# Performance work log

Measured on AMD Instinct MI355X. Metric: run time of the kernel, lower is better.

The kernel has to match this reference:

```python
import jax, jax.numpy as jnp
import numpy as np

# Hard-coded 36-node detector graph from the source (1-indexed), 220 directed edges.
E_SRC = [1,2,3,4,5,6,7,8,9,10,11,12,13,14,15,16,17,18,19,20,21,22,23,24,25,26,27,28,29,30,31,32,33,34,35,36,4,3,8,7,19,20,15,16,35,36,31,32,11,12,11,11,11,12,12,12,6,5,25,26,28,25,9,9,9,10,10,10,1,2,3,4,5,6,7,8,9,10,11,12,13,14,15,16,17,18,17,18,19,20,16,15,31,32,36,35,3,4,7,8,6,5,25,28,14,9,12,11,1,4,2,3,4,1,6,7,8,5,10,11,12,9,14,15,16,13,18,19,20,17,22,23,24,21,26,27,28,25,30,31,32,29,34,35,36,33,33,34,1,2,14,13,30,29,23,22,21,24,22,21,36,33,4,31,30,15,27,28,18,17,10,9,14,19,18,5,8,1,19,20,21,22,23,24,25,26,27,28,29,30,31,32,33,34,35,36,25,26,13,14,30,29,24,21,23,22,33,34,1,2,28,27,10,9,12,15,22,21,11,10]
E_DST = [2,3,4,1,6,7,8,5,10,11,12,9,14,15,16,13,18,19,20,17,22,23,24,21,26,27,28,25,30,31,32,29,34,35,36,33,33,34,1,2,14,13,30,29,23,22,21,24,22,21,36,33,4,31,30,15,27,28,18,17,10,9,14,19,18,5,8,1,19,20,21,22,23,24,25,26,27,28,29,30,31,32,33,34,35,36,25,26,13,14,30,29,24,21,23,22,33,34,1,2,28,27,10,9,12,15,22,21,11,10,1,2,3,4,5,6,7,8,9,10,11,12,13,14,15,16,17,18,19,20,21,22,23,24,25,26,27,28,29,30,31,32,33,34,35,36,4,3,8,7,19,20,15,16,35,36,31,32,11,12,11,11,11,12,12,12,6,5,25,26,28,25,9,9,9,10,10,10,1,2,3,4,5,6,7,8,9,10,11,12,13,14,15,16,17,18,17,18,19,20,16,15,31,32,36,35,3,4,7,8,6,5,25,28,14,9,12,11,1,4]

B = 20000   # graphs per batch
P = 36      # nodes per graph
N = B * P


def setup_inputs() -> dict:
    key = jax.random.key(0)
    ks = jax.random.split(key, 12)
    src = np.asarray(E_SRC, np.int32) - 1
    dst = np.asarray(E_DST, np.int32) - 1
    offs = (np.arange(B, dtype=np.int32) * P)[:, None]
    edge_index = jnp.asarray(np.stack([(src[None, :] + offs).reshape(-1),
                                       (dst[None, :] + offs).reshape(-1)]))  # [2, B*220]
    batch_index = jnp.asarray(np.repeat(np.arange(B, dtype=np.int32), P))  # [N]
    x = jax.random.normal(ks[0], (N, 2), jnp.float32)
    pos = jax.random.normal(ks[1], (N, 3), jnp.float32)  # unused by forward (faithful to source)

    def lin_w(k, fi, fo):
        s = 1.0 / np.sqrt(fi)
        return jax.random.uniform(k, (fi, fo), jnp.float32, -s, s)

    def lin_b(k, fo):
        return jax.random.uniform(k, (fo,), jnp.float32, -0.05, 0.05)

    return {
        "x": x, "edge_index": edge_index, "pos": pos, "batch_index": batch_index,
        "W0": lin_w(ks[2], 2, 4),   "b0": lin_b(ks[3], 4),
        "W1": lin_w(ks[4], 4, 12),  "b1": lin_b(ks[5], 12),
        "W2": lin_w(ks[6], 12, 16), "b2": lin_b(ks[7], 16),
        "W3": lin_w(ks[8], 16, 32), "b3": lin_b(ks[9], 32),
        "Wfc": lin_w(ks[10], 64, 7), "bfc": lin_b(ks[11], 7),
    }


def reference(x, edge_index, pos, batch_index, W0, b0, W1, b1, W2, b2, W3, b3, Wfc, bfc):
    del pos  # present in the torch signature but unused
    src, dst = edge_index[0], edge_index[1]
    n = x.shape[0]
    # GCN symmetric normalization with self-loops: deg = 1 + in-degree
    deg = jax.ops.segment_sum(jnp.ones(src.shape, x.dtype), dst, num_segments=n) + 1.0
    inv = deg ** -0.5
    enorm = inv[src] * inv[dst]   # edge norm
    snorm = inv * inv             # self-loop norm (deg^-1)

    def gcn_conv(h, W, b):
        h = h @ W  # [n, fo]
        agg = jax.ops.segment_sum(h[src] * enorm[:, None], dst, num_segments=n)
        return agg + h * snorm[:, None] + b

    h = jax.nn.relu(gcn_conv(x, W0, b0))
    h = jax.nn.relu(gcn_conv(h, W1, b1))
    # dropout(0.2) is identity in eval mode
    h = jax.nn.relu(gcn_conv(h, W2, b2))
    h = jax.nn.relu(gcn_conv(h, W3, b3))

    gmp = jax.ops.segment_max(h, batch_index, num_segments=B)
    counts = jax.ops.segment_sum(jnp.ones((n,), h.dtype), batch_index, num_segments=B)
    gap = jax.ops.segment_sum(h, batch_index, num_segments=B) / counts[:, None]
    hidden = jnp.concatenate([gmp, gap], axis=1)  # [B, 64]
    out = jax.nn.relu(hidden @ Wfc + bfc)         # [B, 7]
    return (out, hidden)
```

## Files before the change

### kernel.cpp

```cpp
#include <hip/hip_runtime.h>

typedef __attribute__((ext_vector_type(2))) float f32x2;
typedef __attribute__((ext_vector_type(4))) float f32x4;

#define NGRAPH 20000
#define GPB 6
#define STRIDE 36
#define SB (STRIDE * 4)
#define BOFF 64

static __constant__ int c_indeg[36] = {
    7,5,5,7,6,5,5,6,9,9,9,9,5,7,7,5,5,6,6,5,7,7,5,5,7,5,5,7,5,6,6,5,6,5,5,6
};
static __constant__ signed char c_adj[36][9] = {
    {3,7,9,6,1,18,10,0,0},      {0,6,7,2,19,0,0,0,0},
    {1,3,33,32,20,0,0,0,0},     {2,10,0,32,21,33,9,0,0},
    {7,9,5,27,22,26,0,0,0},     {4,6,26,23,27,0,0,0,0},
    {5,7,1,24,0,0,0,0,0},       {6,9,4,0,25,1,0,0,0},
    {11,24,27,9,13,18,17,26,14},{8,27,24,3,10,4,7,0,27},
    {9,0,11,21,35,32,3,28,20},  {10,13,8,20,30,29,14,29,21},
    {15,19,18,13,30,0,0,0,0},   {12,18,8,19,14,31,11,0,0},
    {13,11,8,15,29,32,28,0,0},  {14,12,28,33,29,0,0,0,0},
    {19,25,17,34,24,0,0,0,0},   {16,24,8,18,35,25,0,0,0},
    {17,8,0,19,13,12,0,0,0},    {18,1,16,12,13,0,0,0,0},
    {23,30,11,2,31,10,21,0,0},  {20,35,10,3,34,11,22,0,0},
    {21,34,4,35,23,0,0,0,0},    {22,31,5,30,20,0,0,0,0},
    {27,6,16,25,17,8,9,0,0},    {24,7,17,26,16,0,0,0,0},
    {25,5,8,27,4,0,0,0,0},      {26,4,9,5,24,9,8,0,0},
    {31,15,10,14,29,0,0,0,0},   {28,14,11,11,15,30,0,0,0},
    {29,11,12,31,20,23,0,0,0},  {30,13,28,23,20,0,0,0,0},
    {35,3,10,14,2,33,0,0,0},    {32,2,15,3,34,0,0,0,0},
    {33,16,35,22,21,0,0,0,0},   {34,10,17,32,21,22,0,0,0},
};
static __constant__ float c_inv[36] = {
    0.35355339f,0.40824829f,0.40824829f,0.35355339f,0.37796447f,0.40824829f,
    0.40824829f,0.37796447f,0.31622777f,0.31622777f,0.31622777f,0.31622777f,
    0.40824829f,0.35355339f,0.35355339f,0.40824829f,0.40824829f,0.37796447f,
    0.37796447f,0.40824829f,0.35355339f,0.35355339f,0.40824829f,0.40824829f,
    0.35355339f,0.40824829f,0.40824829f,0.35355339f,0.40824829f,0.37796447f,
    0.37796447f,0.40824829f,0.37796447f,0.40824829f,0.40824829f,0.37796447f,
};

static __device__ __forceinline__ f32x2 relu2(f32x2 v) {
    return __builtin_elementwise_max(v, (f32x2){0.f, 0.f});
}

extern "C" __global__ __launch_bounds__(256, 5)
void gcn_fused(const float* __restrict__ x,
               const float* __restrict__ W0, const float* __restrict__ b0,
               const float* __restrict__ W1, const float* __restrict__ b1,
               const float* __restrict__ W2, const float* __restrict__ b2,
               const float* __restrict__ W3, const float* __restrict__ b3,
               const float* __restrict__ Wfc, const float* __restrict__ bfc,
               float* __restrict__ out)
{
    __shared__ float L[GPB * 36 * STRIDE];

    const int t = threadIdx.x;
    const int g = t / 36;
    const int v = t - g * 36;
    const bool act = (g < GPB);
    const int gq = act ? g : GPB - 1;
    const int vc = act ? v : 0;
    const int G  = blockIdx.x * GPB + g;
    const int Gc = (act && G < NGRAPH) ? G : 0;

    const int nd = c_indeg[vc];
    const float inv_v = c_inv[vc];
    int aoff[9];
#pragma unroll
    for (int k = 0; k < 9; ++k)
        aoff[k] = (gq * 36 + (int)c_adj[vc][k]) * SB;
    float* srow = &L[(gq * 36 + vc) * STRIDE];
    const char* Lb = (const char*)L;

    f32x2 h0a, h0b;
    {
        const float2 xv = ((const float2*)x)[(size_t)Gc * 36 + vc];
        const float s0 = xv.x * inv_v, s1 = xv.y * inv_v;
        if (act) { srow[0] = s0; srow[1] = s1; }
        __syncthreads();
        f32x2 c = {s0, s1};
#pragma unroll
        for (int k = 0; k < 5; ++k) c += *(const f32x2*)(Lb + aoff[k]);
        if (nd > 5) c += *(const f32x2*)(Lb + aoff[5]);
        if (nd > 6) c += *(const f32x2*)(Lb + aoff[6]);
        if (nd > 7) { c += *(const f32x2*)(Lb + aoff[7]);
                      c += *(const f32x2*)(Lb + aoff[8]); }
        const float a0 = c.x * inv_v, a1 = c.y * inv_v;
        const f32x2 a0v = {a0, a0}, a1v = {a1, a1};
        const f32x2* W0v = (const f32x2*)W0;
        const f32x2* b0v = (const f32x2*)b0;
        h0a = relu2(__builtin_elementwise_fma(a0v, W0v[0],
                    __builtin_elementwise_fma(a1v, W0v[2], b0v[0])));
        h0b = relu2(__builtin_elementwise_fma(a0v, W0v[1],
                    __builtin_elementwise_fma(a1v, W0v[3], b0v[1])));
    }

    f32x2 h1[6];
    {
        const f32x2 iv = {inv_v, inv_v};
        const f32x2 s0 = h0a * iv, s1 = h0b * iv;
        if (act) *(f32x4*)&srow[16] = (f32x4){s0.x, s0.y, s1.x, s1.y};
        __syncthreads();
        f32x4 c = {s0.x, s0.y, s1.x, s1.y};
#pragma unroll
        for (int k = 0; k < 5; ++k) c += *(const f32x4*)(Lb + aoff[k] + BOFF);
        if (nd > 5) c += *(const f32x4*)(Lb + aoff[5] + BOFF);
        if (nd > 6) c += *(const f32x4*)(Lb + aoff[6] + BOFF);
        if (nd > 7) { c += *(const f32x4*)(Lb + aoff[7] + BOFF);
                      c += *(const f32x4*)(Lb + aoff[8] + BOFF); }
        float a[4];
#pragma unroll
        for (int i = 0; i < 4; ++i) a[i] = c[i] * inv_v;
        f32x2 z[6];
        const f32x2* b1v = (const f32x2*)b1;
#pragma unroll
        for (int j = 0; j < 6; ++j) z[j] = b1v[j];
        const f32x2* W1v = (const f32x2*)W1;
#pragma unroll
        for (int i = 0; i < 4; ++i) {
            const f32x2 av = {a[i], a[i]};
#pragma unroll
            for (int j = 0; j < 6; ++j)
                z[j] = __builtin_elementwise_fma(av, W1v[i * 6 + j], z[j]);
        }
#pragma unroll
        for (int j = 0; j < 6; ++j) h1[j] = relu2(z[j]);
    }

    f32x2 h2[8];
    {
        const f32x2 iv = {inv_v, inv_v};
        f32x2 s[6];
#pragma unroll
        for (int j = 0; j < 6; ++j) s[j] = h1[j] * iv;
        if (act) {
            *(f32x4*)&srow[0] = (f32x4){s[0].x, s[0].y, s[1].x, s[1].y};
            *(f32x4*)&srow[4] = (f32x4){s[2].x, s[2].y, s[3].x, s[3].y};
            *(f32x4*)&srow[8] = (f32x4){s[4].x, s[4].y, s[5].x, s[5].y};
        }
        __syncthreads();
        f32x4 c0 = {s[0].x, s[0].y, s[1].x, s[1].y};
        f32x4 c1 = {s[2].x, s[2].y, s[3].x, s[3].y};
        f32x4 c2 = {s[4].x, s[4].y, s[5].x, s[5].y};
#pragma unroll
        for (int k = 0; k < 5; ++k) {
            const char* base = Lb + aoff[k];
            c0 += *(const f32x4*)(base);
            c1 += *(const f32x4*)(base + 16);
            c2 += *(const f32x4*)(base + 32);
        }
        if (nd > 5) { const char* base = Lb + aoff[5];
            c0 += *(const f32x4*)(base); c1 += *(const f32x4*)(base + 16);
            c2 += *(const f32x4*)(base + 32); }
        if (nd > 6) { const char* base = Lb + aoff[6];
            c0 += *(const f32x4*)(base); c1 += *(const f32x4*)(base + 16);
            c2 += *(const f32x4*)(base + 32); }
        if (nd > 7) {
            const char* ba = Lb + aoff[7];
            c0 += *(const f32x4*)(ba); c1 += *(const f32x4*)(ba + 16);
            c2 += *(const f32x4*)(ba + 32);
            const char* bb = Lb + aoff[8];
            c0 += *(const f32x4*)(bb); c1 += *(const f32x4*)(bb + 16);
            c2 += *(const f32x4*)(bb + 32);
        }
        float a[12];
#pragma unroll
        for (int i = 0; i < 4; ++i) {
            a[i] = c0[i] * inv_v; a[4 + i] = c1[i] * inv_v; a[8 + i] = c2[i] * inv_v;
        }
        f32x2 z[8];
        const f32x2* b2v = (const f32x2*)b2;
#pragma unroll
        for (int j = 0; j < 8; ++j) z[j] = b2v[j];
        const f32x2* W2v = (const f32x2*)W2;
#pragma unroll
        for (int i = 0; i < 12; ++i) {
            const f32x2 av = {a[i], a[i]};
#pragma unroll
            for (int j = 0; j < 8; ++j)
                z[j] = __builtin_elementwise_fma(av, W2v[i * 8 + j], z[j]);
        }
#pragma unroll
        for (int j = 0; j < 8; ++j) h2[j] = relu2(z[j]);
    }

    f32x2 h3[16];
    {
        const f32x2 iv = {inv_v, inv_v};
        f32x2 s[8];
#pragma unroll
        for (int j = 0; j < 8; ++j) s[j] = h2[j] * iv;
        if (act) {
#pragma unroll
            for (int q = 0; q < 4; ++q)
                *(f32x4*)&srow[16 + q * 4] =
                    (f32x4){s[2*q].x, s[2*q].y, s[2*q+1].x, s[2*q+1].y};
        }
        __syncthreads();
        f32x4 c0 = {s[0].x, s[0].y, s[1].x, s[1].y};
        f32x4 c1 = {s[2].x, s[2].y, s[3].x, s[3].y};
        f32x4 c2 = {s[4].x, s[4].y, s[5].x, s[5].y};
        f32x4 c3 = {s[6].x, s[6].y, s[7].x, s[7].y};
#pragma unroll
        for (int k = 0; k < 5; ++k) {
            const char* base = Lb + aoff[k] + BOFF;
            c0 += *(const f32x4*)(base);      c1 += *(const f32x4*)(base + 16);
            c2 += *(const f32x4*)(base + 32); c3 += *(const f32x4*)(base + 48);
        }
        if (nd > 5) { const char* base = Lb + aoff[5] + BOFF;
            c0 += *(const f32x4*)(base);      c1 += *(const f32x4*)(base + 16);
            c2 += *(const f32x4*)(base + 32); c3 += *(const f32x4*)(base + 48); }
        if (nd > 6) { const char* base = Lb + aoff[6] + BOFF;
            c0 += *(const f32x4*)(base);      c1 += *(const f32x4*)(base + 16);
            c2 += *(const f32x4*)(base + 32); c3 += *(const f32x4*)(base + 48); }
        if (nd > 7) {
            const char* ba = Lb + aoff[7] + BOFF;
            c0 += *(const f32x4*)(ba);      c1 += *(const f32x4*)(ba + 16);
            c2 += *(const f32x4*)(ba + 32); c3 += *(const f32x4*)(ba + 48);
            const char* bb = Lb + aoff[8] + BOFF;
            c0 += *(const f32x4*)(bb);      c1 += *(const f32x4*)(bb + 16);
            c2 += *(const f32x4*)(bb + 32); c3 += *(const f32x4*)(bb + 48);
        }
        float a[16];
#pragma unroll
        for (int i = 0; i < 4; ++i) {
            a[i] = c0[i] * inv_v;      a[4 + i] = c1[i] * inv_v;
            a[8 + i] = c2[i] * inv_v;  a[12 + i] = c3[i] * inv_v;
        }
        f32x2 z[16];
        const f32x2* b3v = (const f32x2*)b3;
#pragma unroll
        for (int j = 0; j < 16; ++j) z[j] = b3v[j];
        const f32x2* W3v = (const f32x2*)W3;
#pragma unroll
        for (int i = 0; i < 16; ++i) {
            const f32x2 av = {a[i], a[i]};
#pragma unroll
            for (int j = 0; j < 16; ++j)
                z[j] = __builtin_elementwise_fma(av, W3v[i * 16 + j], z[j]);
        }
#pragma unroll
        for (int j = 0; j < 16; ++j) h3[j] = relu2(z[j]);
    }

    if (act) {
#pragma unroll
        for (int q = 0; q < 4; ++q)
            *(f32x4*)&srow[q * 4] =
                (f32x4){h3[2*q].x, h3[2*q].y, h3[2*q+1].x, h3[2*q+1].y};
    }
    __syncthreads();
    if (act) {
#pragma unroll
        for (int q = 0; q < 4; ++q)
            *(f32x4*)&srow[16 + q * 4] =
                (f32x4){h3[8+2*q].x, h3[8+2*q].y, h3[9+2*q].x, h3[9+2*q].y};
    }
    __syncthreads();

    if (t < GPB * 32) {
        const int pg = t >> 5, pf = t & 31;
        const int PG = blockIdx.x * GPB + pg;
        const float* col = &L[(pg * 36) * STRIDE + pf];
        float mx = -1e30f, sm = 0.f;
#pragma unroll
        for (int u = 0; u < 36; ++u) {
            const float val = col[u * STRIDE];
            mx = fmaxf(mx, val); sm += val;
        }
        const float gap = sm * (1.0f / 36.0f);
        if (PG < NGRAPH) {
            float* ho = out + (size_t)NGRAPH * 7 + (size_t)PG * 64;
            ho[pf] = mx; ho[32 + pf] = gap;
        }
        float p[7];
        const float* wr0 = Wfc + pf * 7;
        const float* wr1 = Wfc + (32 + pf) * 7;
#pragma unroll
        for (int o = 0; o < 7; ++o)
            p[o] = fmaf(mx, wr0[o], gap * wr1[o]);
#pragma unroll
        for (int m = 16; m >= 1; m >>= 1) {
#pragma unroll
            for (int o = 0; o < 7; ++o)
                p[o] += __shfl_xor(p[o], m, 32);
        }
        if (pf < 7 && PG < NGRAPH) {
            float w = p[0];
            w = (pf == 1) ? p[1] : w;
            w = (pf == 2) ? p[2] : w;
            w = (pf == 3) ? p[3] : w;
            w = (pf == 4) ? p[4] : w;
            w = (pf == 5) ? p[5] : w;
            w = (pf == 6) ? p[6] : w;
            out[(size_t)PG * 7 + pf] = fmaxf(w + bfc[pf], 0.f);
        }
    }
}

extern "C" void kernel_launch(void* const* d_in, const int* in_sizes, int n_in,
                              void* d_out, int out_size, void* d_ws, size_t ws_size,
                              hipStream_t stream) {
    (void)in_sizes; (void)n_in; (void)d_ws; (void)ws_size; (void)out_size;
    const float* x   = (const float*)d_in[0];
    const float* W0  = (const float*)d_in[4];
    const float* b0  = (const float*)d_in[5];
    const float* W1  = (const float*)d_in[6];
    const float* b1  = (const float*)d_in[7];
    const float* W2  = (const float*)d_in[8];
    const float* b2  = (const float*)d_in[9];
    const float* W3  = (const float*)d_in[10];
    const float* b3  = (const float*)d_in[11];
    const float* Wfc = (const float*)d_in[12];
    const float* bfc = (const float*)d_in[13];
    float* out = (float*)d_out;

    const int nblocks = (NGRAPH + GPB - 1) / GPB;
    hipLaunchKernelGGL(gcn_fused, dim3(nblocks), dim3(256), 0, stream,
                       x, W0, b0, W1, b1, W2, b2, W3, b3, Wfc, bfc, out);
}
```

Before: 35.77 us.

## Pack seven graphs per block and aggregate layer 0 from global memory

Each block now handles seven graphs (252 of 256 threads) instead of six, and the launch-bounds occupancy hint drops from 5 to 4. The first layer's neighbour aggregation now reads the neighbours' x values straight from global memory with a per-edge precomputed normalisation table. This removes one LDS write and one barrier. The shared-memory column offsets are reshuffled to match, the adjacency row is loaded as packed words, and the pooling loop is unrolled by two. In exchange the kernel does more scattered global loads, and the lower occupancy hint may limit latency hiding.

```diff
diff --git a/kernel.cpp b/kernel.cpp
--- a/kernel.cpp
+++ b/kernel.cpp
@@ -4,10 +4,9 @@
 typedef __attribute__((ext_vector_type(4))) float f32x4;
 
 #define NGRAPH 20000
-#define GPB 6
+#define GPB 7
 #define STRIDE 36
 #define SB (STRIDE * 4)
-#define BOFF 64
 
 static __constant__ int c_indeg[36] = {
     7,5,5,7,6,5,5,6,9,9,9,9,5,7,7,5,5,6,6,5,7,7,5,5,7,5,5,7,5,6,6,5,6,5,5,6
@@ -40,12 +39,36 @@
     0.35355339f,0.40824829f,0.40824829f,0.35355339f,0.40824829f,0.37796447f,
     0.37796447f,0.40824829f,0.37796447f,0.40824829f,0.40824829f,0.37796447f,
 };
+#define A_ 0.35355339f
+#define B_ 0.40824829f
+#define C_ 0.37796447f
+#define D_ 0.31622777f
+static __constant__ float c_ninv[36][9] = {
+    {A_,C_,D_,B_,B_,C_,D_,0,0}, {A_,B_,C_,B_,B_,0,0,0,0},
+    {B_,A_,B_,C_,A_,0,0,0,0},   {B_,D_,A_,C_,A_,B_,D_,0,0},
+    {C_,D_,B_,A_,B_,B_,0,0,0},  {C_,B_,B_,B_,A_,0,0,0,0},
+    {B_,C_,B_,A_,A_,0,0,0,0},   {B_,D_,C_,A_,B_,B_,0,0,0},
+    {D_,A_,A_,D_,A_,C_,C_,B_,A_},{D_,A_,A_,A_,D_,C_,C_,A_,A_},
+    {D_,A_,D_,A_,C_,C_,A_,B_,A_},{D_,A_,D_,A_,C_,C_,A_,C_,A_},
+    {B_,B_,C_,A_,C_,0,0,0,0},   {B_,C_,D_,B_,A_,B_,D_,0,0},
+    {A_,D_,D_,B_,C_,C_,B_,0,0}, {A_,B_,B_,B_,C_,0,0,0,0},
+    {B_,B_,C_,B_,A_,0,0,0,0},   {B_,A_,D_,C_,C_,B_,0,0,0},
+    {C_,D_,A_,B_,A_,B_,0,0,0},  {C_,B_,B_,B_,A_,0,0,0,0},
+    {B_,C_,D_,B_,B_,D_,A_,0,0}, {A_,C_,D_,A_,B_,D_,B_,0,0},
+    {A_,B_,C_,C_,B_,0,0,0,0},   {B_,B_,B_,C_,A_,0,0,0,0},
+    {A_,B_,B_,B_,C_,D_,D_,0,0}, {A_,C_,C_,B_,B_,0,0,0,0},
+    {B_,B_,D_,A_,C_,0,0,0,0},   {B_,C_,D_,B_,A_,D_,D_,0,0},
+    {B_,B_,D_,A_,C_,0,0,0,0},   {B_,A_,D_,D_,B_,C_,0,0,0},
+    {C_,D_,B_,B_,A_,B_,0,0,0},  {C_,A_,B_,B_,A_,0,0,0,0},
+    {C_,A_,D_,A_,B_,B_,0,0,0},  {C_,B_,B_,A_,B_,0,0,0,0},
+    {B_,B_,C_,B_,A_,0,0,0,0},   {B_,D_,C_,C_,A_,B_,0,0,0},
+};
 
 static __device__ __forceinline__ f32x2 relu2(f32x2 v) {
     return __builtin_elementwise_max(v, (f32x2){0.f, 0.f});
 }
 
-extern "C" __global__ __launch_bounds__(256, 5)
+extern "C" __global__ __launch_bounds__(256, 4)
 void gcn_fused(const float* __restrict__ x,
                const float* __restrict__ W0, const float* __restrict__ b0,
                const float* __restrict__ W1, const float* __restrict__ b1,
@@ -67,27 +90,47 @@
 
     const int nd = c_indeg[vc];
     const float inv_v = c_inv[vc];
-    int aoff[9];
-#pragma unroll
-    for (int k = 0; k < 9; ++k)
-        aoff[k] = (gq * 36 + (int)c_adj[vc][k]) * SB;
+    int nb[9], aoff[9];
+    {
+        const unsigned char* ar = (const unsigned char*)&c_adj[vc][0];
+        const unsigned int w0 = *(const unsigned int*)(ar);
+        const unsigned int w1 = *(const unsigned int*)(ar + 4);
+        const unsigned int w2 = *(const unsigned int*)(ar + 8);
+#pragma unroll
+        for (int k = 0; k < 4; ++k) nb[k] = (int)((w0 >> (8 * k)) & 0xff);
+#pragma unroll
+        for (int k = 0; k < 4; ++k) nb[4 + k] = (int)((w1 >> (8 * k)) & 0xff);
+        nb[8] = (int)(w2 & 0xff);
+#pragma unroll
+        for (int k = 0; k < 9; ++k) aoff[k] = (gq * 36 + nb[k]) * SB;
+    }
     float* srow = &L[(gq * 36 + vc) * STRIDE];
     const char* Lb = (const char*)L;
 
     f32x2 h0a, h0b;
     {
-        const float2 xv = ((const float2*)x)[(size_t)Gc * 36 + vc];
-        const float s0 = xv.x * inv_v, s1 = xv.y * inv_v;
-        if (act) { srow[0] = s0; srow[1] = s1; }
-        __syncthreads();
-        f32x2 c = {s0, s1};
-#pragma unroll
-        for (int k = 0; k < 5; ++k) c += *(const f32x2*)(Lb + aoff[k]);
-        if (nd > 5) c += *(const f32x2*)(Lb + aoff[5]);
-        if (nd > 6) c += *(const f32x2*)(Lb + aoff[6]);
-        if (nd > 7) { c += *(const f32x2*)(Lb + aoff[7]);
-                      c += *(const f32x2*)(Lb + aoff[8]); }
-        const float a0 = c.x * inv_v, a1 = c.y * inv_v;
+        const float2* x2 = (const float2*)x;
+        const int xb = Gc * 36;
+        const float2 xs = x2[xb + vc];
+        f32x2 acc = {xs.x * inv_v, xs.y * inv_v};
+        const float* nr = &c_ninv[vc][0];
+#pragma unroll
+        for (int k = 0; k < 5; ++k) {
+            const float2 xu = x2[xb + nb[k]];
+            const float w = nr[k];
+            acc.x = fmaf(w, xu.x, acc.x); acc.y = fmaf(w, xu.y, acc.y);
+        }
+        if (nd > 5) { const float2 xu = x2[xb + nb[5]]; const float w = nr[5];
+            acc.x = fmaf(w, xu.x, acc.x); acc.y = fmaf(w, xu.y, acc.y); }
+        if (nd > 6) { const float2 xu = x2[xb + nb[6]]; const float w = nr[6];
+            acc.x = fmaf(w, xu.x, acc.x); acc.y = fmaf(w, xu.y, acc.y); }
+        if (nd > 7) {
+            const float2 xu7 = x2[xb + nb[7]]; const float w7 = nr[7];
+            acc.x = fmaf(w7, xu7.x, acc.x); acc.y = fmaf(w7, xu7.y, acc.y);
+            const float2 xu8 = x2[xb + nb[8]]; const float w8 = nr[8];
+            acc.x = fmaf(w8, xu8.x, acc.x); acc.y = fmaf(w8, xu8.y, acc.y);
+        }
+        const float a0 = acc.x * inv_v, a1 = acc.y * inv_v;
         const f32x2 a0v = {a0, a0}, a1v = {a1, a1};
         const f32x2* W0v = (const f32x2*)W0;
         const f32x2* b0v = (const f32x2*)b0;
@@ -101,15 +144,15 @@
     {
         const f32x2 iv = {inv_v, inv_v};
         const f32x2 s0 = h0a * iv, s1 = h0b * iv;
-        if (act) *(f32x4*)&srow[16] = (f32x4){s0.x, s0.y, s1.x, s1.y};
+        if (act) *(f32x4*)&srow[0] = (f32x4){s0.x, s0.y, s1.x, s1.y};
         __syncthreads();
         f32x4 c = {s0.x, s0.y, s1.x, s1.y};
 #pragma unroll
-        for (int k = 0; k < 5; ++k) c += *(const f32x4*)(Lb + aoff[k] + BOFF);
-        if (nd > 5) c += *(const f32x4*)(Lb + aoff[5] + BOFF);
-        if (nd > 6) c += *(const f32x4*)(Lb + aoff[6] + BOFF);
-        if (nd > 7) { c += *(const f32x4*)(Lb + aoff[7] + BOFF);
-                      c += *(const f32x4*)(Lb + aoff[8] + BOFF); }
+        for (int k = 0; k < 5; ++k) c += *(const f32x4*)(Lb + aoff[k]);
+        if (nd > 5) c += *(const f32x4*)(Lb + aoff[5]);
+        if (nd > 6) c += *(const f32x4*)(Lb + aoff[6]);
+        if (nd > 7) { c += *(const f32x4*)(Lb + aoff[7]);
+                      c += *(const f32x4*)(Lb + aoff[8]); }
         float a[4];
 #pragma unroll
         for (int i = 0; i < 4; ++i) a[i] = c[i] * inv_v;
@@ -136,9 +179,9 @@
 #pragma unroll
         for (int j = 0; j < 6; ++j) s[j] = h1[j] * iv;
         if (act) {
-            *(f32x4*)&srow[0] = (f32x4){s[0].x, s[0].y, s[1].x, s[1].y};
-            *(f32x4*)&srow[4] = (f32x4){s[2].x, s[2].y, s[3].x, s[3].y};
-            *(f32x4*)&srow[8] = (f32x4){s[4].x, s[4].y, s[5].x, s[5].y};
+            *(f32x4*)&srow[4]  = (f32x4){s[0].x, s[0].y, s[1].x, s[1].y};
+            *(f32x4*)&srow[8]  = (f32x4){s[2].x, s[2].y, s[3].x, s[3].y};
+            *(f32x4*)&srow[12] = (f32x4){s[4].x, s[4].y, s[5].x, s[5].y};
         }
         __syncthreads();
         f32x4 c0 = {s[0].x, s[0].y, s[1].x, s[1].y};
@@ -146,22 +189,22 @@
         f32x4 c2 = {s[4].x, s[4].y, s[5].x, s[5].y};
 #pragma unroll
         for (int k = 0; k < 5; ++k) {
-            const char* base = Lb + aoff[k];
+            const char* base = Lb + aoff[k] + 16;
             c0 += *(const f32x4*)(base);
             c1 += *(const f32x4*)(base + 16);
             c2 += *(const f32x4*)(base + 32);
         }
-        if (nd > 5) { const char* base = Lb + aoff[5];
+        if (nd > 5) { const char* base = Lb + aoff[5] + 16;
             c0 += *(const f32x4*)(base); c1 += *(const f32x4*)(base + 16);
             c2 += *(const f32x4*)(base + 32); }
-        if (nd > 6) { const char* base = Lb + aoff[6];
+        if (nd > 6) { const char* base = Lb + aoff[6] + 16;
             c0 += *(const f32x4*)(base); c1 += *(const f32x4*)(base + 16);
             c2 += *(const f32x4*)(base + 32); }
         if (nd > 7) {
-            const char* ba = Lb + aoff[7];
+            const char* ba = Lb + aoff[7] + 16;
             c0 += *(const f32x4*)(ba); c1 += *(const f32x4*)(ba + 16);
             c2 += *(const f32x4*)(ba + 32);
-            const char* bb = Lb + aoff[8];
+            const char* bb = Lb + aoff[8] + 16;
             c0 += *(const f32x4*)(bb); c1 += *(const f32x4*)(bb + 16);
             c2 += *(const f32x4*)(bb + 32);
         }
@@ -205,21 +248,21 @@
         f32x4 c3 = {s[6].x, s[6].y, s[7].x, s[7].y};
 #pragma unroll
         for (int k = 0; k < 5; ++k) {
-            const char* base = Lb + aoff[k] + BOFF;
+            const char* base = Lb + aoff[k] + 64;
             c0 += *(const f32x4*)(base);      c1 += *(const f32x4*)(base + 16);
             c2 += *(const f32x4*)(base + 32); c3 += *(const f32x4*)(base + 48);
         }
-        if (nd > 5) { const char* base = Lb + aoff[5] + BOFF;
+        if (nd > 5) { const char* base = Lb + aoff[5] + 64;
             c0 += *(const f32x4*)(base);      c1 += *(const f32x4*)(base + 16);
             c2 += *(const f32x4*)(base + 32); c3 += *(const f32x4*)(base + 48); }
-        if (nd > 6) { const char* base = Lb + aoff[6] + BOFF;
+        if (nd > 6) { const char* base = Lb + aoff[6] + 64;
             c0 += *(const f32x4*)(base);      c1 += *(const f32x4*)(base + 16);
             c2 += *(const f32x4*)(base + 32); c3 += *(const f32x4*)(base + 48); }
         if (nd > 7) {
-            const char* ba = Lb + aoff[7] + BOFF;
+            const char* ba = Lb + aoff[7] + 64;
             c0 += *(const f32x4*)(ba);      c1 += *(const f32x4*)(ba + 16);
             c2 += *(const f32x4*)(ba + 32); c3 += *(const f32x4*)(ba + 48);
-            const char* bb = Lb + aoff[8] + BOFF;
+            const char* bb = Lb + aoff[8] + 64;
             c0 += *(const f32x4*)(bb);      c1 += *(const f32x4*)(bb + 16);
             c2 += *(const f32x4*)(bb + 32); c3 += *(const f32x4*)(bb + 48);
         }
@@ -266,9 +309,10 @@
         const float* col = &L[(pg * 36) * STRIDE + pf];
         float mx = -1e30f, sm = 0.f;
 #pragma unroll
-        for (int u = 0; u < 36; ++u) {
-            const float val = col[u * STRIDE];
-            mx = fmaxf(mx, val); sm += val;
+        for (int u = 0; u < 18; ++u) {
+            const float v0 = col[0], v1 = col[STRIDE];
+            mx = fmaxf(mx, fmaxf(v0, v1)); sm += v0 + v1;
+            col += 2 * STRIDE;
         }
         const float gap = sm * (1.0f / 36.0f);
         if (PG < NGRAPH) {
```

New measurement: 36.40 us. No clear change (+1.7%).

## Process two interleaved graph streams per thread with seven graphs per stream

Applied to the files above, without the earlier changes.

Each thread now handles one node in two separate graphs (stream A and stream B), and each block packs 7 graphs per stream instead of 6, so every block covers 14 graphs. This raises thread utilization (252 of 256 threads active) and gives each thread independent instruction streams to hide LDS and FMA latency. Weight loads are now shared across the two graphs. The cost is doubled register and LDS use per block, with launch bounds lowered to 2 blocks per CU, so occupancy drops. The LDS row layout is also reshuffled to fit the larger feature slices.

```diff
diff --git a/kernel.cpp b/kernel.cpp
--- a/kernel.cpp
+++ b/kernel.cpp
@@ -4,10 +4,11 @@
 typedef __attribute__((ext_vector_type(4))) float f32x4;
 
 #define NGRAPH 20000
-#define GPB 6
+#define GPT 7
 #define STRIDE 36
 #define SB (STRIDE * 4)
-#define BOFF 64
+#define BSTREAM (GPT * 36 * STRIDE)
+#define BSTREAMB (BSTREAM * 4)
 
 static __constant__ int c_indeg[36] = {
     7,5,5,7,6,5,5,6,9,9,9,9,5,7,7,5,5,6,6,5,7,7,5,5,7,5,5,7,5,6,6,5,6,5,5,6
@@ -45,7 +46,59 @@
     return __builtin_elementwise_max(v, (f32x2){0.f, 0.f});
 }
 
-extern "C" __global__ __launch_bounds__(256, 5)
+static __device__ __forceinline__ void xf1(const float* a, const float* W1,
+                                           const float* b1, f32x2* h) {
+    f32x2 z[6];
+    const f32x2* bv = (const f32x2*)b1;
+#pragma unroll
+    for (int j = 0; j < 6; ++j) z[j] = bv[j];
+    const f32x2* Wv = (const f32x2*)W1;
+#pragma unroll
+    for (int i = 0; i < 4; ++i) {
+        const f32x2 av = {a[i], a[i]};
+#pragma unroll
+        for (int j = 0; j < 6; ++j)
+            z[j] = __builtin_elementwise_fma(av, Wv[i * 6 + j], z[j]);
+    }
+#pragma unroll
+    for (int j = 0; j < 6; ++j) h[j] = relu2(z[j]);
+}
+static __device__ __forceinline__ void xf2(const float* a, const float* W2,
+                                           const float* b2, f32x2* h) {
+    f32x2 z[8];
+    const f32x2* bv = (const f32x2*)b2;
+#pragma unroll
+    for (int j = 0; j < 8; ++j) z[j] = bv[j];
+    const f32x2* Wv = (const f32x2*)W2;
+#pragma unroll
+    for (int i = 0; i < 12; ++i) {
+        const f32x2 av = {a[i], a[i]};
+#pragma unroll
+        for (int j = 0; j < 8; ++j)
+            z[j] = __builtin_elementwise_fma(av, Wv[i * 8 + j], z[j]);
+    }
+#pragma unroll
+    for (int j = 0; j < 8; ++j) h[j] = relu2(z[j]);
+}
+static __device__ __forceinline__ void xf3(const float* a, const float* W3,
+                                           const float* b3, f32x2* h) {
+    f32x2 z[16];
+    const f32x2* bv = (const f32x2*)b3;
+#pragma unroll
+    for (int j = 0; j < 16; ++j) z[j] = bv[j];
+    const f32x2* Wv = (const f32x2*)W3;
+#pragma unroll
+    for (int i = 0; i < 16; ++i) {
+        const f32x2 av = {a[i], a[i]};
+#pragma unroll
+        for (int j = 0; j < 16; ++j)
+            z[j] = __builtin_elementwise_fma(av, Wv[i * 16 + j], z[j]);
+    }
+#pragma unroll
+    for (int j = 0; j < 16; ++j) h[j] = relu2(z[j]);
+}
+
+extern "C" __global__ __launch_bounds__(256, 2)
 void gcn_fused(const float* __restrict__ x,
                const float* __restrict__ W0, const float* __restrict__ b0,
                const float* __restrict__ W1, const float* __restrict__ b1,
@@ -54,248 +107,302 @@
                const float* __restrict__ Wfc, const float* __restrict__ bfc,
                float* __restrict__ out)
 {
-    __shared__ float L[GPB * 36 * STRIDE];
+    __shared__ float L[2 * BSTREAM];
 
     const int t = threadIdx.x;
     const int g = t / 36;
     const int v = t - g * 36;
-    const bool act = (g < GPB);
-    const int gq = act ? g : GPB - 1;
+    const bool act = (g < GPT);
+    const int gq = act ? g : GPT - 1;
     const int vc = act ? v : 0;
-    const int G  = blockIdx.x * GPB + g;
-    const int Gc = (act && G < NGRAPH) ? G : 0;
+    const int GA = blockIdx.x * (2 * GPT) + g;
+    const int GB = GA + GPT;
+    const int GcA = (act && GA < NGRAPH) ? GA : 0;
+    const int GcB = (act && GB < NGRAPH) ? GB : 0;
+    const bool okB = (GB < NGRAPH);
 
     const int nd = c_indeg[vc];
     const float inv_v = c_inv[vc];
-    int aoff[9];
-#pragma unroll
-    for (int k = 0; k < 9; ++k)
+    int aoff[9], boff[9];
+#pragma unroll
+    for (int k = 0; k < 9; ++k) {
         aoff[k] = (gq * 36 + (int)c_adj[vc][k]) * SB;
-    float* srow = &L[(gq * 36 + vc) * STRIDE];
+        boff[k] = aoff[k] + BSTREAMB;
+    }
+    float* srowA = &L[(gq * 36 + vc) * STRIDE];
+    float* srowB = srowA + BSTREAM;
     const char* Lb = (const char*)L;
 
-    f32x2 h0a, h0b;
+    f32x2 h0A[2], h0B[2];
     {
-        const float2 xv = ((const float2*)x)[(size_t)Gc * 36 + vc];
-        const float s0 = xv.x * inv_v, s1 = xv.y * inv_v;
-        if (act) { srow[0] = s0; srow[1] = s1; }
+        const float2* x2 = (const float2*)x;
+        const float2 xA = x2[(size_t)GcA * 36 + vc];
+        const float2 xB = x2[(size_t)GcB * 36 + vc];
+        const f32x2 sA = {xA.x * inv_v, xA.y * inv_v};
+        const f32x2 sB = {xB.x * inv_v, xB.y * inv_v};
+        if (act) { *(f32x2*)&srowA[32] = sA; *(f32x2*)&srowB[32] = sB; }
         __syncthreads();
-        f32x2 c = {s0, s1};
-#pragma unroll
-        for (int k = 0; k < 5; ++k) c += *(const f32x2*)(Lb + aoff[k]);
-        if (nd > 5) c += *(const f32x2*)(Lb + aoff[5]);
-        if (nd > 6) c += *(const f32x2*)(Lb + aoff[6]);
-        if (nd > 7) { c += *(const f32x2*)(Lb + aoff[7]);
-                      c += *(const f32x2*)(Lb + aoff[8]); }
-        const float a0 = c.x * inv_v, a1 = c.y * inv_v;
-        const f32x2 a0v = {a0, a0}, a1v = {a1, a1};
+        f32x2 cA = sA, cB = sB;
+#pragma unroll
+        for (int k = 0; k < 5; ++k) {
+            cA += *(const f32x2*)(Lb + aoff[k] + 128);
+            cB += *(const f32x2*)(Lb + boff[k] + 128);
+        }
+        if (nd > 5) { cA += *(const f32x2*)(Lb + aoff[5] + 128);
+                      cB += *(const f32x2*)(Lb + boff[5] + 128); }
+        if (nd > 6) { cA += *(const f32x2*)(Lb + aoff[6] + 128);
+                      cB += *(const f32x2*)(Lb + boff[6] + 128); }
+        if (nd > 7) { cA += *(const f32x2*)(Lb + aoff[7] + 128);
+                      cB += *(const f32x2*)(Lb + boff[7] + 128);
+                      cA += *(const f32x2*)(Lb + aoff[8] + 128);
+                      cB += *(const f32x2*)(Lb + boff[8] + 128); }
         const f32x2* W0v = (const f32x2*)W0;
         const f32x2* b0v = (const f32x2*)b0;
-        h0a = relu2(__builtin_elementwise_fma(a0v, W0v[0],
-                    __builtin_elementwise_fma(a1v, W0v[2], b0v[0])));
-        h0b = relu2(__builtin_elementwise_fma(a0v, W0v[1],
-                    __builtin_elementwise_fma(a1v, W0v[3], b0v[1])));
-    }
-
-    f32x2 h1[6];
+        {
+            const float a0 = cA.x * inv_v, a1 = cA.y * inv_v;
+            const f32x2 a0v = {a0, a0}, a1v = {a1, a1};
+            h0A[0] = relu2(__builtin_elementwise_fma(a0v, W0v[0],
+                     __builtin_elementwise_fma(a1v, W0v[2], b0v[0])));
+            h0A[1] = relu2(__builtin_elementwise_fma(a0v, W0v[1],
+                     __builtin_elementwise_fma(a1v, W0v[3], b0v[1])));
+        }
+        {
+            const float a0 = cB.x * inv_v, a1 = cB.y * inv_v;
+            const f32x2 a0v = {a0, a0}, a1v = {a1, a1};
+            h0B[0] = relu2(__builtin_elementwise_fma(a0v, W0v[0],
+                     __builtin_elementwise_fma(a1v, W0v[2], b0v[0])));
+            h0B[1] = relu2(__builtin_elementwise_fma(a0v, W0v[1],
+                     __builtin_elementwise_fma(a1v, W0v[3], b0v[1])));
+        }
+    }
+
+    f32x2 h1A[6], h1B[6];
     {
         const f32x2 iv = {inv_v, inv_v};
-        const f32x2 s0 = h0a * iv, s1 = h0b * iv;
-        if (act) *(f32x4*)&srow[16] = (f32x4){s0.x, s0.y, s1.x, s1.y};
+        const f32x2 sA0 = h0A[0] * iv, sA1 = h0A[1] * iv;
+        const f32x2 sB0 = h0B[0] * iv, sB1 = h0B[1] * iv;
+        if (act) {
+            *(f32x4*)&srowA[0] = (f32x4){sA0.x, sA0.y, sA1.x, sA1.y};
+            *(f32x4*)&srowB[0] = (f32x4){sB0.x, sB0.y, sB1.x, sB1.y};
+        }
         __syncthreads();
-        f32x4 c = {s0.x, s0.y, s1.x, s1.y};
-#pragma unroll
-        for (int k = 0; k < 5; ++k) c += *(const f32x4*)(Lb + aoff[k] + BOFF);
-        if (nd > 5) c += *(const f32x4*)(Lb + aoff[5] + BOFF);
-        if (nd > 6) c += *(const f32x4*)(Lb + aoff[6] + BOFF);
-        if (nd > 7) { c += *(const f32x4*)(Lb + aoff[7] + BOFF);
-                      c += *(const f32x4*)(Lb + aoff[8] + BOFF); }
-        float a[4];
-#pragma unroll
-        for (int i = 0; i < 4; ++i) a[i] = c[i] * inv_v;
-        f32x2 z[6];
-        const f32x2* b1v = (const f32x2*)b1;
-#pragma unroll
-        for (int j = 0; j < 6; ++j) z[j] = b1v[j];
-        const f32x2* W1v = (const f32x2*)W1;
-#pragma unroll
-        for (int i = 0; i < 4; ++i) {
-            const f32x2 av = {a[i], a[i]};
-#pragma unroll
-            for (int j = 0; j < 6; ++j)
-                z[j] = __builtin_elementwise_fma(av, W1v[i * 6 + j], z[j]);
-        }
-#pragma unroll
-        for (int j = 0; j < 6; ++j) h1[j] = relu2(z[j]);
-    }
-
-    f32x2 h2[8];
+        f32x4 cA = {sA0.x, sA0.y, sA1.x, sA1.y};
+        f32x4 cB = {sB0.x, sB0.y, sB1.x, sB1.y};
+#pragma unroll
+        for (int k = 0; k < 5; ++k) {
+            cA += *(const f32x4*)(Lb + aoff[k]);
+            cB += *(const f32x4*)(Lb + boff[k]);
+        }
+        if (nd > 5) { cA += *(const f32x4*)(Lb + aoff[5]);
+                      cB += *(const f32x4*)(Lb + boff[5]); }
+        if (nd > 6) { cA += *(const f32x4*)(Lb + aoff[6]);
+                      cB += *(const f32x4*)(Lb + boff[6]); }
+        if (nd > 7) { cA += *(const f32x4*)(Lb + aoff[7]);
+                      cB += *(const f32x4*)(Lb + boff[7]);
+                      cA += *(const f32x4*)(Lb + aoff[8]);
+                      cB += *(const f32x4*)(Lb + boff[8]); }
+        float aA[4], aB[4];
+#pragma unroll
+        for (int i = 0; i < 4; ++i) { aA[i] = cA[i] * inv_v; aB[i] = cB[i] * inv_v; }
+        xf1(aA, W1, b1, h1A);
+        xf1(aB, W1, b1, h1B);
+    }
+
+    f32x2 h2A[8], h2B[8];
     {
         const f32x2 iv = {inv_v, inv_v};
-        f32x2 s[6];
-#pragma unroll
-        for (int j = 0; j < 6; ++j) s[j] = h1[j] * iv;
+        f32x2 sA[6], sB[6];
+#pragma unroll
+        for (int j = 0; j < 6; ++j) { sA[j] = h1A[j] * iv; sB[j] = h1B[j] * iv; }
         if (act) {
-            *(f32x4*)&srow[0] = (f32x4){s[0].x, s[0].y, s[1].x, s[1].y};
-            *(f32x4*)&srow[4] = (f32x4){s[2].x, s[2].y, s[3].x, s[3].y};
-            *(f32x4*)&srow[8] = (f32x4){s[4].x, s[4].y, s[5].x, s[5].y};
+            *(f32x4*)&srowA[4]  = (f32x4){sA[0].x, sA[0].y, sA[1].x, sA[1].y};
+            *(f32x4*)&srowA[8]  = (f32x4){sA[2].x, sA[2].y, sA[3].x, sA[3].y};
+            *(f32x4*)&srowA[12] = (f32x4){sA[4].x, sA[4].y, sA[5].x, sA[5].y};
+            *(f32x4*)&srowB[4]  = (f32x4){sB[0].x, sB[0].y, sB[1].x, sB[1].y};
+            *(f32x4*)&srowB[8]  = (f32x4){sB[2].x, sB[2].y, sB[3].x, sB[3].y};
+            *(f32x4*)&srowB[12] = (f32x4){sB[4].x, sB[4].y, sB[5].x, sB[5].y};
         }
         __syncthreads();
-        f32x4 c0 = {s[0].x, s[0].y, s[1].x, s[1].y};
-        f32x4 c1 = {s[2].x, s[2].y, s[3].x, s[3].y};
-        f32x4 c2 = {s[4].x, s[4].y, s[5].x, s[5].y};
+        f32x4 cA0 = {sA[0].x, sA[0].y, sA[1].x, sA[1].y};
+        f32x4 cA1 = {sA[2].x, sA[2].y, sA[3].x, sA[3].y};
+        f32x4 cA2 = {sA[4].x, sA[4].y, sA[5].x, sA[5].y};
+        f32x4 cB0 = {sB[0].x, sB[0].y, sB[1].x, sB[1].y};
+        f32x4 cB1 = {sB[2].x, sB[2].y, sB[3].x, sB[3].y};
+        f32x4 cB2 = {sB[4].x, sB[4].y, sB[5].x, sB[5].y};
 #pragma unroll
         for (int k = 0; k < 5; ++k) {
-            const char* base = Lb + aoff[k];
-            c0 += *(const f32x4*)(base);
-            c1 += *(const f32x4*)(base + 16);
-            c2 += *(const f32x4*)(base + 32);
-        }
-        if (nd > 5) { const char* base = Lb + aoff[5];
-            c0 += *(const f32x4*)(base); c1 += *(const f32x4*)(base + 16);
-            c2 += *(const f32x4*)(base + 32); }
-        if (nd > 6) { const char* base = Lb + aoff[6];
-            c0 += *(const f32x4*)(base); c1 += *(const f32x4*)(base + 16);
-            c2 += *(const f32x4*)(base + 32); }
+            const char* pa = Lb + aoff[k] + 16;
+            const char* pb = Lb + boff[k] + 16;
+            cA0 += *(const f32x4*)(pa);      cB0 += *(const f32x4*)(pb);
+            cA1 += *(const f32x4*)(pa + 16); cB1 += *(const f32x4*)(pb + 16);
+            cA2 += *(const f32x4*)(pa + 32); cB2 += *(const f32x4*)(pb + 32);
+        }
+        if (nd > 5) { const char* pa = Lb + aoff[5] + 16; const char* pb = Lb + boff[5] + 16;
+            cA0 += *(const f32x4*)(pa);      cB0 += *(const f32x4*)(pb);
+            cA1 += *(const f32x4*)(pa + 16); cB1 += *(const f32x4*)(pb + 16);
+            cA2 += *(const f32x4*)(pa + 32); cB2 += *(const f32x4*)(pb + 32); }
+        if (nd > 6) { const char* pa = Lb + aoff[6] + 16; const char* pb = Lb + boff[6] + 16;
+            cA0 += *(const f32x4*)(pa);      cB0 += *(const f32x4*)(pb);
+            cA1 += *(const f32x4*)(pa + 16); cB1 += *(const f32x4*)(pb + 16);
+            cA2 += *(const f32x4*)(pa + 32); cB2 += *(const f32x4*)(pb + 32); }
         if (nd > 7) {
-            const char* ba = Lb + aoff[7];
-            c0 += *(const f32x4*)(ba); c1 += *(const f32x4*)(ba + 16);
-            c2 += *(const f32x4*)(ba + 32);
-            const char* bb = Lb + aoff[8];
-            c0 += *(const f32x4*)(bb); c1 += *(const f32x4*)(bb + 16);
-            c2 += *(const f32x4*)(bb + 32);
-        }
-        float a[12];
+            const char* pa = Lb + aoff[7] + 16; const char* pb = Lb + boff[7] + 16;
+            cA0 += *(const f32x4*)(pa);      cB0 += *(const f32x4*)(pb);
+            cA1 += *(const f32x4*)(pa + 16); cB1 += *(const f32x4*)(pb + 16);
+            cA2 += *(const f32x4*)(pa + 32); cB2 += *(const f32x4*)(pb + 32);
+            const char* qa = Lb + aoff[8] + 16; const char* qb = Lb + boff[8] + 16;
+            cA0 += *(const f32x4*)(qa);      cB0 += *(const f32x4*)(qb);
+            cA1 += *(const f32x4*)(qa + 16); cB1 += *(const f32x4*)(qb + 16);
+            cA2 += *(const f32x4*)(qa + 32); cB2 += *(const f32x4*)(qb + 32);
+        }
+        float aA[12], aB[12];
 #pragma unroll
         for (int i = 0; i < 4; ++i) {
-            a[i] = c0[i] * inv_v; a[4 + i] = c1[i] * inv_v; a[8 + i] = c2[i] * inv_v;
-        }
-        f32x2 z[8];
-        const f32x2* b2v = (const f32x2*)b2;
-#pragma unroll
-        for (int j = 0; j < 8; ++j) z[j] = b2v[j];
-        const f32x2* W2v = (const f32x2*)W2;
-#pragma unroll
-        for (int i = 0; i < 12; ++i) {
-            const f32x2 av = {a[i], a[i]};
-#pragma unroll
-            for (int j = 0; j < 8; ++j)
-                z[j] = __builtin_elementwise_fma(av, W2v[i * 8 + j], z[j]);
-        }
-#pragma unroll
-        for (int j = 0; j < 8; ++j) h2[j] = relu2(z[j]);
-    }
-
-    f32x2 h3[16];
+            aA[i] = cA0[i] * inv_v; aA[4+i] = cA1[i] * inv_v; aA[8+i] = cA2[i] * inv_v;
+            aB[i] = cB0[i] * inv_v; aB[4+i] = cB1[i] * inv_v; aB[8+i] = cB2[i] * inv_v;
+        }
+        xf2(aA, W2, b2, h2A);
+        xf2(aB, W2, b2, h2B);
+    }
+
+    f32x2 h3A[16], h3B[16];
     {
         const f32x2 iv = {inv_v, inv_v};
-        f32x2 s[8];
-#pragma unroll
-        for (int j = 0; j < 8; ++j) s[j] = h2[j] * iv;
+        f32x2 sA[8], sB[8];
+#pragma unroll
+        for (int j = 0; j < 8; ++j) { sA[j] = h2A[j] * iv; sB[j] = h2B[j] * iv; }
         if (act) {
 #pragma unroll
-            for (int q = 0; q < 4; ++q)
-                *(f32x4*)&srow[16 + q * 4] =
-                    (f32x4){s[2*q].x, s[2*q].y, s[2*q+1].x, s[2*q+1].y};
+            for (int q = 0; q < 4; ++q) {
+                *(f32x4*)&srowA[16 + q*4] =
+                    (f32x4){sA[2*q].x, sA[2*q].y, sA[2*q+1].x, sA[2*q+1].y};
+                *(f32x4*)&srowB[16 + q*4] =
+                    (f32x4){sB[2*q].x, sB[2*q].y, sB[2*q+1].x, sB[2*q+1].y};
+            }
         }
         __syncthreads();
-        f32x4 c0 = {s[0].x, s[0].y, s[1].x, s[1].y};
-        f32x4 c1 = {s[2].x, s[2].y, s[3].x, s[3].y};
-        f32x4 c2 = {s[4].x, s[4].y, s[5].x, s[5].y};
-        f32x4 c3 = {s[6].x, s[6].y, s[7].x, s[7].y};
+        f32x4 cA0 = {sA[0].x, sA[0].y, sA[1].x, sA[1].y};
+        f32x4 cA1 = {sA[2].x, sA[2].y, sA[3].x, sA[3].y};
+        f32x4 cA2 = {sA[4].x, sA[4].y, sA[5].x, sA[5].y};
+        f32x4 cA3 = {sA[6].x, sA[6].y, sA[7].x, sA[7].y};
+        f32x4 cB0 = {sB[0].x, sB[0].y, sB[1].x, sB[1].y};
+        f32x4 cB1 = {sB[2].x, sB[2].y, sB[3].x, sB[3].y};
+        f32x4 cB2 = {sB[4].x, sB[4].y, sB[5].x, sB[5].y};
+        f32x4 cB3 = {sB[6].x, sB[6].y, sB[7].x, sB[7].y};
 #pragma unroll
         for (int k = 0; k < 5; ++k) {
-            const char* base = Lb + aoff[k] + BOFF;
-            c0 += *(const f32x4*)(base);      c1 += *(const f32x4*)(base + 16);
-            c2 += *(const f32x4*)(base + 32); c3 += *(const f32x4*)(base + 48);
-        }
-        if (nd > 5) { const char* base = Lb + aoff[5] + BOFF;
-            c0 += *(const f32x4*)(base);      c1 += *(const f32x4*)(base + 16);
-            c2 += *(const f32x4*)(base + 32); c3 += *(const f32x4*)(base + 48); }
-        if (nd > 6) { const char* base = Lb + aoff[6] + BOFF;
-            c0 += *(const f32x4*)(base);      c1 += *(const f32x4*)(base + 16);
-            c2 += *(const f32x4*)(base + 32); c3 += *(const f32x4*)(base + 48); }
+            const char* pa = Lb + aoff[k] + 64;
+            const char* pb = Lb + boff[k] + 64;
+            cA0 += *(const f32x4*)(pa);      cB0 += *(const f32x4*)(pb);
+            cA1 += *(const f32x4*)(pa + 16); cB1 += *(const f32x4*)(pb + 16);
+            cA2 += *(const f32x4*)(pa + 32); cB2 += *(const f32x4*)(pb + 32);
+            cA3 += *(const f32x4*)(pa + 48); cB3 += *(const f32x4*)(pb + 48);
+        }
+        if (nd > 5) { const char* pa = Lb + aoff[5] + 64; const char* pb = Lb + boff[5] + 64;
+            cA0 += *(const f32x4*)(pa);      cB0 += *(const f32x4*)(pb);
+            cA1 += *(const f32x4*)(pa + 16); cB1 += *(const f32x4*)(pb + 16);
+            cA2 += *(const f32x4*)(pa + 32); cB2 += *(const f32x4*)(pb + 32);
+            cA3 += *(const f32x4*)(pa + 48); cB3 += *(const f32x4*)(pb + 48); }
+        if (nd > 6) { const char* pa = Lb + aoff[6] + 64; const char* pb = Lb + boff[6] + 64;
+            cA0 += *(const f32x4*)(pa);      cB0 += *(const f32x4*)(pb);
+            cA1 += *(const f32x4*)(pa + 16); cB1 += *(const f32x4*)(pb + 16);
+            cA2 += *(const f32x4*)(pa + 32); cB2 += *(const f32x4*)(pb + 32);
+            cA3 += *(const f32x4*)(pa + 48); cB3 += *(const f32x4*)(pb + 48); }
         if (nd > 7) {
-            const char* ba = Lb + aoff[7] + BOFF;
-            c0 += *(const f32x4*)(ba);      c1 += *(const f32x4*)(ba + 16);
-            c2 += *(const f32x4*)(ba + 32); c3 += *(const f32x4*)(ba + 48);
-            const char* bb = Lb + aoff[8] + BOFF;
-            c0 += *(const f32x4*)(bb);      c1 += *(const f32x4*)(bb + 16);
-            c2 += *(const f32x4*)(bb + 32); c3 += *(const f32x4*)(bb + 48);
-        }
-        float a[16];
+            const char* pa = Lb + aoff[7] + 64; const char* pb = Lb + boff[7] + 64;
+            cA0 += *(const f32x4*)(pa);      cB0 += *(const f32x4*)(pb);
+            cA1 += *(const f32x4*)(pa + 16); cB1 += *(const f32x4*)(pb + 16);
+            cA2 += *(const f32x4*)(pa + 32); cB2 += *(const f32x4*)(pb + 32);
+            cA3 += *(const f32x4*)(pa + 48); cB3 += *(const f32x4*)(pb + 48);
+            const char* qa = Lb + aoff[8] + 64; const char* qb = Lb + boff[8] + 64;
+            cA0 += *(const f32x4*)(qa);      cB0 += *(const f32x4*)(qb);
+            cA1 += *(const f32x4*)(qa + 16); cB1 += *(const f32x4*)(qb + 16);
+            cA2 += *(const f32x4*)(qa + 32); cB2 += *(const f32x4*)(qb + 32);
+            cA3 += *(const f32x4*)(qa + 48); cB3 += *(const f32x4*)(qb + 48);
+        }
+        float aA[16], aB[16];
 #pragma unroll
         for (int i = 0; i < 4; ++i) {
-            a[i] = c0[i] * inv_v;      a[4 + i] = c1[i] * inv_v;
-            a[8 + i] = c2[i] * inv_v;  a[12 + i] = c3[i] * inv_v;
-        }
-        f32x2 z[16];
-        const f32x2* b3v = (const f32x2*)b3;
-#pragma unroll
-        for (int j = 0; j < 16; ++j) z[j] = b3v[j];
-        const f32x2* W3v = (const f32x2*)W3;
-#pragma unroll
-        for (int i = 0; i < 16; ++i) {
-            const f32x2 av = {a[i], a[i]};
-#pragma unroll
-            for (int j = 0; j < 16; ++j)
-                z[j] = __builtin_elementwise_fma(av, W3v[i * 16 + j], z[j]);
-        }
-#pragma unroll
-        for (int j = 0; j < 16; ++j) h3[j] = relu2(z[j]);
+            aA[i] = cA0[i] * inv_v; aA[4+i]  = cA1[i] * inv_v;
+            aA[8+i] = cA2[i] * inv_v; aA[12+i] = cA3[i] * inv_v;
+            aB[i] = cB0[i] * inv_v; aB[4+i]  = cB1[i] * inv_v;
+            aB[8+i] = cB2[i] * inv_v; aB[12+i] = cB3[i] * inv_v;
+        }
+        xf3(aA, W3, b3, h3A);
+        xf3(aB, W3, b3, h3B);
     }
 
     if (act) {
-#pragma unroll
-        for (int q = 0; q < 4; ++q)
-            *(f32x4*)&srow[q * 4] =
-                (f32x4){h3[2*q].x, h3[2*q].y, h3[2*q+1].x, h3[2*q+1].y};
+        *(f32x4*)&srowA[0] = (f32x4){h3A[0].x, h3A[0].y, h3A[1].x, h3A[1].y};
+        *(f32x4*)&srowA[4] = (f32x4){h3A[2].x, h3A[2].y, h3A[3].x, h3A[3].y};
+        *(f32x4*)&srowA[8] = (f32x4){h3A[4].x, h3A[4].y, h3A[5].x, h3A[5].y};
+        *(f32x4*)&srowB[0] = (f32x4){h3B[0].x, h3B[0].y, h3B[1].x, h3B[1].y};
+        *(f32x4*)&srowB[4] = (f32x4){h3B[2].x, h3B[2].y, h3B[3].x, h3B[3].y};
+        *(f32x4*)&srowB[8] = (f32x4){h3B[4].x, h3B[4].y, h3B[5].x, h3B[5].y};
     }
     __syncthreads();
     if (act) {
 #pragma unroll
-        for (int q = 0; q < 4; ++q)
-            *(f32x4*)&srow[16 + q * 4] =
-                (f32x4){h3[8+2*q].x, h3[8+2*q].y, h3[9+2*q].x, h3[9+2*q].y};
+        for (int q = 0; q < 5; ++q) {
+            *(f32x4*)&srowA[12 + q*4] =
+                (f32x4){h3A[6+2*q].x, h3A[6+2*q].y, h3A[7+2*q].x, h3A[7+2*q].y};
+            *(f32x4*)&srowB[12 + q*4] =
+                (f32x4){h3B[6+2*q].x, h3B[6+2*q].y, h3B[7+2*q].x, h3B[7+2*q].y};
+        }
     }
     __syncthreads();
 
-    if (t < GPB * 32) {
+    if (t < GPT * 32) {
         const int pg = t >> 5, pf = t & 31;
-        const int PG = blockIdx.x * GPB + pg;
-        const float* col = &L[(pg * 36) * STRIDE + pf];
-        float mx = -1e30f, sm = 0.f;
+        const int PA = blockIdx.x * (2 * GPT) + pg;
+        const int PB = PA + GPT;
+        const float* colA = &L[(pg * 36) * STRIDE + pf];
+        const float* colB = colA + BSTREAM;
+        float mxA = -1e30f, smA = 0.f, mxB = -1e30f, smB = 0.f;
 #pragma unroll
         for (int u = 0; u < 36; ++u) {
-            const float val = col[u * STRIDE];
-            mx = fmaxf(mx, val); sm += val;
-        }
-        const float gap = sm * (1.0f / 36.0f);
-        if (PG < NGRAPH) {
-            float* ho = out + (size_t)NGRAPH * 7 + (size_t)PG * 64;
-            ho[pf] = mx; ho[32 + pf] = gap;
-        }
-        float p[7];
+            const float vA = colA[u * STRIDE];
+            const float vB = colB[u * STRIDE];
+            mxA = fmaxf(mxA, vA); smA += vA;
+            mxB = fmaxf(mxB, vB); smB += vB;
+        }
+        const float gapA = smA * (1.0f / 36.0f);
+        const float gapB = smB * (1.0f / 36.0f);
+        {
+            float* ho = out + (size_t)NGRAPH * 7 + (size_t)PA * 64;
+            ho[pf] = mxA; ho[32 + pf] = gapA;
+        }
+        if (PB < NGRAPH) {
+            float* ho = out + (size_t)NGRAPH * 7 + (size_t)PB * 64;
+            ho[pf] = mxB; ho[32 + pf] = gapB;
+        }
+        float pA[7], pB[7];
         const float* wr0 = Wfc + pf * 7;
         const float* wr1 = Wfc + (32 + pf) * 7;
 #pragma unroll
-        for (int o = 0; o < 7; ++o)
-            p[o] = fmaf(mx, wr0[o], gap * wr1[o]);
+        for (int o = 0; o < 7; ++o) {
+            pA[o] = fmaf(mxA, wr0[o], gapA * wr1[o]);
+            pB[o] = fmaf(mxB, wr0[o], gapB * wr1[o]);
+        }
 #pragma unroll
         for (int m = 16; m >= 1; m >>= 1) {
 #pragma unroll
-            for (int o = 0; o < 7; ++o)
-                p[o] += __shfl_xor(p[o], m, 32);
-        }
-        if (pf < 7 && PG < NGRAPH) {
-            float w = p[0];
-            w = (pf == 1) ? p[1] : w;
-            w = (pf == 2) ? p[2] : w;
-            w = (pf == 3) ? p[3] : w;
-            w = (pf == 4) ? p[4] : w;
-            w = (pf == 5) ? p[5] : w;
-            w = (pf == 6) ? p[6] : w;
-            out[(size_t)PG * 7 + pf] = fmaxf(w + bfc[pf], 0.f);
+            for (int o = 0; o < 7; ++o) {
+                pA[o] += __shfl_xor(pA[o], m, 32);
+                pB[o] += __shfl_xor(pB[o], m, 32);
+            }
+        }
+        if (pf < 7) {
+            float wA = pA[0], wB = pB[0];
+            wA = (pf == 1) ? pA[1] : wA;  wB = (pf == 1) ? pB[1] : wB;
+            wA = (pf == 2) ? pA[2] : wA;  wB = (pf == 2) ? pB[2] : wB;
+            wA = (pf == 3) ? pA[3] : wA;  wB = (pf == 3) ? pB[3] : wB;
+            wA = (pf == 4) ? pA[4] : wA;  wB = (pf == 4) ? pB[4] : wB;
+            wA = (pf == 5) ? pA[5] : wA;  wB = (pf == 5) ? pB[5] : wB;
+            wA = (pf == 6) ? pA[6] : wA;  wB = (pf == 6) ? pB[6] : wB;
+            out[(size_t)PA * 7 + pf] = fmaxf(wA + bfc[pf], 0.f);
+            if (PB < NGRAPH)
+                out[(size_t)PB * 7 + pf] = fmaxf(wB + bfc[pf], 0.f);
         }
     }
 }
@@ -317,7 +424,7 @@
     const float* bfc = (const float*)d_in[13];
     float* out = (float*)d_out;
 
-    const int nblocks = (NGRAPH + GPB - 1) / GPB;
+    const int nblocks = (NGRAPH + 2 * GPT - 1) / (2 * GPT);
     hipLaunchKernelGGL(gcn_fused, dim3(nblocks), dim3(256), 0, stream,
                        x, W0, b0, W1, b1, W2, b2, W3, b3, Wfc, bfc, out);
 }
```

Result: slower. 40.99 us (+14.6%).
